# Kernel optimization log

Hardware: AMD Instinct MI355X
Metric: run time of the kernel (lower is better)

## Reference

```python
import jax, jax.numpy as jnp
import numpy as np

D_MODEL = 1024
N_HEADS = 16
D_K = D_MODEL // N_HEADS
MAX_REL = 128
SCALE = float(np.sqrt(D_K))


def setup_inputs() -> dict:
    key = jax.random.key(0)
    ks = jax.random.split(key, 10)
    B, S = 8, 1024
    return {
        "query": jax.random.normal(ks[0], (B, S, D_MODEL), jnp.float32),
        "key": jax.random.normal(ks[1], (B, S, D_MODEL), jnp.float32),
        "value": jax.random.normal(ks[2], (B, S, D_MODEL), jnp.float32),
        "w_q": jax.random.normal(ks[3], (D_MODEL, D_MODEL), jnp.float32) * (1.0 / np.sqrt(D_MODEL)),
        "w_k": jax.random.normal(ks[4], (D_MODEL, D_MODEL), jnp.float32) * (1.0 / np.sqrt(D_MODEL)),
        "w_v": jax.random.normal(ks[5], (D_MODEL, D_MODEL), jnp.float32) * (1.0 / np.sqrt(D_MODEL)),
        "w_o": jax.random.normal(ks[6], (D_MODEL, D_MODEL), jnp.float32) * (1.0 / np.sqrt(D_MODEL)),
        "b_o": jnp.zeros((D_MODEL,), jnp.float32),
        "rel_k": jax.random.normal(ks[7], (2 * MAX_REL + 1, D_K), jnp.float32),
        "rel_v": jax.random.normal(ks[8], (2 * MAX_REL + 1, D_K), jnp.float32),
        "temporal_decay": jnp.ones((N_HEADS,), jnp.float32),
    }


def reference(query, key, value, w_q, w_k, w_v, w_o, b_o, rel_k, rel_v, temporal_decay):
    B, S, D = query.shape
    H, dk = N_HEADS, D_K
    # projections (torch Linear: x @ W.T), reshape to [B,H,S,dk]
    def proj(x, W):
        return (x @ W.T).reshape(B, S, H, dk).transpose(0, 2, 1, 3)
    Q = proj(query, w_q)
    K = proj(key, w_k)
    V = proj(value, w_v)
    scores = jnp.einsum('bhld,bhrd->bhlr', Q, K) / SCALE
    # relative position indices [S,S] in [0, 2*MAX_REL]
    pos = jnp.arange(S)
    rel_idx = jnp.clip(pos[None, :] - pos[:, None], -MAX_REL, MAX_REL) + MAX_REL
    rp_k = rel_k[rel_idx]  # [S,S,dk]
    scores = scores + jnp.einsum('bhld,lrd->bhlr', Q, rp_k)
    # temporal decay bias
    time_dist = jnp.abs(pos[None, :] - pos[:, None]).astype(scores.dtype)  # [S,S]
    scores = scores - temporal_decay[None, :, None, None] * time_dist[None, None]
    attn = jax.nn.softmax(scores, axis=-1)
    context = jnp.einsum('bhlr,bhrd->bhld', attn, V)
    rp_v = rel_v[rel_idx]  # [S,S,dk]
    context = context + jnp.einsum('bhlr,lrd->bhld', attn, rp_v)
    context = context.transpose(0, 2, 1, 3).reshape(B, S, D)
    output = context @ w_o.T + b_o
    return output, attn
```

## Files before the change

### kernel.cpp

```cpp
#include <hip/hip_runtime.h>
#include <cstdint>
#include <cstddef>

#define S_LEN 1024
#define DMODEL 1024
#define NHEADS 16
#define DK 64
#define BATCH 8
#define PUS 296
#define PBS 272
#define RELS 257
#define SLABS 68

using half8_t  = __attribute__((ext_vector_type(8))) _Float16;
using half4_t  = __attribute__((ext_vector_type(4))) _Float16;
using float4_t = __attribute__((ext_vector_type(4))) float;

__device__ __forceinline__ void async16(const void* g, void* l) {
  __builtin_amdgcn_global_load_lds(
      (const __attribute__((address_space(1))) unsigned int*)g,
      (__attribute__((address_space(3))) unsigned int*)l, 16, 0, 0);
}

struct CvtRegion { const float* src; _Float16* dst; int n4; float scale; };
struct CvtArgs { CvtRegion r[8]; };

__global__ __launch_bounds__(256) void cvt_all_kernel(CvtArgs a) {
  CvtRegion reg = a.r[blockIdx.y];
  const int stride = gridDim.x * 256;
  for (int i = blockIdx.x * 256 + threadIdx.x; i < reg.n4; i += stride) {
    float4_t f = ((const float4_t*)reg.src)[i];
    half4_t h;
    h[0] = (_Float16)(f[0] * reg.scale); h[1] = (_Float16)(f[1] * reg.scale);
    h[2] = (_Float16)(f[2] * reg.scale); h[3] = (_Float16)(f[3] * reg.scale);
    ((half4_t*)reg.dst)[i] = h;
  }
}

__global__ void build_rvT_kernel(const float* __restrict__ relv, _Float16* __restrict__ rvT) {
  int d = blockIdx.x;
  int j = threadIdx.x;
  rvT[d * 256 + j] = (j < 255) ? (_Float16)relv[(size_t)(j + 1) * DK + d] : (_Float16)0.f;
}

__device__ __forceinline__ void gemm_core(
    const _Float16* __restrict__ A, const _Float16* __restrict__ B,
    _Float16* smem, float4_t acc[4][4], int m0, int n0,
    int wave, int lane, int quad, int ln, int wm, int wn)
{
  _Float16* As = smem;
  _Float16* Bs = smem + 8192;
#pragma unroll
  for (int i = 0; i < 4; i++)
#pragma unroll
    for (int j = 0; j < 4; j++) { acc[i][j][0]=0.f; acc[i][j][1]=0.f; acc[i][j][2]=0.f; acc[i][j][3]=0.f; }

  for (int k0 = 0; k0 < 1024; k0 += 64) {
#pragma unroll
    for (int q = 0; q < 4; q++) {
      int slot = q * 256 + wave * 64 + lane;
      int m = slot >> 3, g = slot & 7;
      int gg = g ^ (m & 7);
      async16(A + (size_t)(m0 + m) * 1024 + k0 + gg * 8,
              As + (size_t)(q * 256 + wave * 64) * 8);
      async16(B + (size_t)(n0 + m) * 1024 + k0 + gg * 8,
              Bs + (size_t)(q * 256 + wave * 64) * 8);
    }
    __syncthreads();
    half8_t af[4][2], bf[4][2];
#pragma unroll
    for (int t = 0; t < 4; t++) {
      int mm = wm + t * 16 + ln;
      int nn = wn + t * 16 + ln;
#pragma unroll
      for (int kk = 0; kk < 2; kk++) {
        af[t][kk] = *(const half8_t*)(As + mm * 64 + (((kk * 4 + quad) ^ (mm & 7)) * 8));
        bf[t][kk] = *(const half8_t*)(Bs + nn * 64 + (((kk * 4 + quad) ^ (nn & 7)) * 8));
      }
    }
#pragma unroll
    for (int i = 0; i < 4; i++)
#pragma unroll
      for (int j = 0; j < 4; j++) {
        acc[i][j] = __builtin_amdgcn_mfma_f32_16x16x32_f16(af[i][0], bf[j][0], acc[i][j], 0, 0, 0);
        acc[i][j] = __builtin_amdgcn_mfma_f32_16x16x32_f16(af[i][1], bf[j][1], acc[i][j], 0, 0, 0);
      }
    __syncthreads();
  }
}

struct QkvArgs {
  const _Float16* A[3];
  const _Float16* B[3];
  _Float16* dst[3];
};

__global__ __launch_bounds__(256) void gemm_qkv(QkvArgs qa) {
  __shared__ _Float16 smem[16384];
  const int tid = threadIdx.x;
  const int wave = tid >> 6, lane = tid & 63;
  const int quad = lane >> 4, ln = lane & 15;
  const int m0 = blockIdx.x * 128, n0 = blockIdx.y * 128;
  const int wm = (wave >> 1) * 64, wn = (wave & 1) * 64;
  const int z = blockIdx.z;

  float4_t acc[4][4];
  gemm_core(qa.A[z], qa.B[z], smem, acc, m0, n0, wave, lane, quad, ln, wm, wn);

  _Float16* o = qa.dst[z];
  if (z < 2) {
    _Float16* T = smem + wave * 1152;
    size_t headoff = ((size_t)((n0 + wn) >> 6)) << 16;
#pragma unroll
    for (int i = 0; i < 4; i++) {
#pragma unroll
      for (int j = 0; j < 4; j++)
#pragma unroll
        for (int r = 0; r < 4; r++)
          T[(quad * 4 + r) * 72 + j * 16 + ln] = (_Float16)acc[i][j][r];
      int mbase = m0 + wm + i * 16;
#pragma unroll
      for (int p = 0; p < 2; p++) {
        int row = p * 8 + (lane >> 3);
        int cc = (lane & 7) * 8;
        half8_t hv = *(const half8_t*)(T + row * 72 + cc);
        int token = mbase + row;
        size_t idx = ((size_t)(token >> 10) << 20) | headoff
                   | ((size_t)(token & 1023) << 6) | (size_t)cc;
        *(half8_t*)(o + idx) = hv;
      }
    }
  } else {
    _Float16* T = smem + wave * 1160;
    const int tok0 = m0 + wm;
    const size_t base = ((size_t)(tok0 >> 10) << 20)
                      | (((size_t)((n0 + wn) >> 6)) << 16)
                      | (size_t)(tok0 & 1023);
#pragma unroll
    for (int j = 0; j < 4; j++) {
#pragma unroll
      for (int i = 0; i < 4; i++)
#pragma unroll
        for (int r = 0; r < 4; r++)
          T[ln * 72 + i * 16 + quad * 4 + r] = (_Float16)acc[i][j][r];
#pragma unroll
      for (int p = 0; p < 2; p++) {
        int drow = p * 8 + (lane >> 3);
        int cc = (lane & 7) * 8;
        half8_t hv = *(const half8_t*)(T + drow * 72 + cc);
        size_t idx = base + (((size_t)(j * 16 + drow)) << 10) + (size_t)cc;
        *(half8_t*)(o + idx) = hv;
      }
    }
  }
}

__global__ __launch_bounds__(256) void gemm_out(
    const _Float16* __restrict__ A, const _Float16* __restrict__ B,
    float* __restrict__ o, const float* __restrict__ bias)
{
  __shared__ _Float16 smem[16384];
  const int tid = threadIdx.x;
  const int wave = tid >> 6, lane = tid & 63;
  const int quad = lane >> 4, ln = lane & 15;
  const int m0 = blockIdx.x * 128, n0 = blockIdx.y * 128;
  const int wm = (wave >> 1) * 64, wn = (wave & 1) * 64;

  float4_t acc[4][4];
  gemm_core(A, B, smem, acc, m0, n0, wave, lane, quad, ln, wm, wn);

#pragma unroll
  for (int i = 0; i < 4; i++)
#pragma unroll
    for (int j = 0; j < 4; j++) {
      int nn = n0 + wn + j * 16 + ln;
      float bb = bias[nn];
#pragma unroll
      for (int r = 0; r < 4; r++) {
        int mm = m0 + wm + i * 16 + quad * 4 + r;
        o[(size_t)mm * 1024 + nn] = acc[i][j][r] + bb;
      }
    }
}

__global__ __launch_bounds__(256, 4) void attn4_kernel(
    const _Float16* __restrict__ Qh, const _Float16* __restrict__ Kh,
    const _Float16* __restrict__ VtG, const _Float16* __restrict__ relk,
    const _Float16* __restrict__ rvT, const float* __restrict__ decay,
    float* __restrict__ attn_out, _Float16* __restrict__ ctx)
{
  __shared__ float    scratch[4 * 16 * SLABS];
  __shared__ _Float16 Pu[16 * PUS];
  __shared__ _Float16 Pband[16 * PBS];
  __shared__ float    statsM[4][16];
  __shared__ float    statsZ[4][16];

  const int tid = threadIdx.x;
  const int wave = tid >> 6, lane = tid & 63;
  const int quad = lane >> 4, ln = lane & 15;
  const int hw = blockIdx.x;
  const int bid = ((hw & 7) << 10) | (hw >> 3);
  const int b = bid >> 10, h = (bid >> 6) & 15, lt = bid & 63;
  const int l0 = lt * 16;
  const int bh = b * NHEADS + h;
  const _Float16* Qb = Qh + ((size_t)bh << 16);
  const _Float16* Kb = Kh + ((size_t)bh << 16);
  const _Float16* Vb = VtG + ((size_t)bh << 16);
  float* arow = attn_out + ((size_t)bh << 20) + (size_t)l0 * S_LEN;
  const float dec = decay[h];

  const int rlo = (l0 > 127) ? ((l0 - 127) & ~15) : 0;
  int rhi = (l0 + 158) & ~15;
  if (rhi > S_LEN) rhi = S_LEN;
  const int W = rhi - rlo;
  const int nT = W >> 4;
  const int ts = (wave * nT) >> 2;
  const int te = ((wave + 1) * nT) >> 2;

  const float4_t fz = {0.f, 0.f, 0.f, 0.f};
  {
    int w4l = rlo >> 2;
    int w4r = (S_LEN - rhi) >> 2;
#pragma unroll 1
    for (int row = 0; row < 16; row++) {
      float* ar = arow + (size_t)row * S_LEN;
      for (int c4 = tid; c4 < w4l; c4 += 256)
        __builtin_nontemporal_store(fz, (float4_t*)(ar + c4 * 4));
      float* ar2 = ar + rhi;
      for (int c4 = tid; c4 < w4r; c4 += 256)
        __builtin_nontemporal_store(fz, (float4_t*)(ar2 + c4 * 4));
    }
  }
  {
    const half8_t hz = {};
    for (int i = tid; i < 16 * PBS / 8; i += 256) ((half8_t*)Pband)[i] = hz;
    for (int i = tid; i < 16 * PUS / 8; i += 256) ((half8_t*)Pu)[i] = hz;
  }

  half8_t aq[2];
  {
    const _Float16* qp = Qb + (size_t)(l0 + ln) * DK + quad * 8;
    aq[0] = *(const half8_t*)(qp);
    aq[1] = *(const half8_t*)(qp + 32);
  }

#pragma unroll
  for (int s = 0; s < 4; s++) {
    int nt = wave * 4 + s;
    int j = nt * 16 + ln;
    const _Float16* bp = relk + (size_t)(j + 1) * DK + quad * 8;
    half8_t b0 = *(const half8_t*)bp;
    half8_t b1 = *(const half8_t*)(bp + 32);
    float4_t c = {0.f, 0.f, 0.f, 0.f};
    c = __builtin_amdgcn_mfma_f32_16x16x32_f16(aq[0], b0, c, 0, 0, 0);
    c = __builtin_amdgcn_mfma_f32_16x16x32_f16(aq[1], b1, c, 0, 0, 0);
    float db = dec * fabsf((float)(j - 127));
#pragma unroll
    for (int i = 0; i < 4; i++) scratch[(quad * 4 + i) * RELS + j] = c[i] - db;
  }
  __syncthreads();

  float4_t sreg[5];
#pragma unroll
  for (int tt = 0; tt < 5; tt++) { sreg[tt][0]=-1e30f; sreg[tt][1]=-1e30f; sreg[tt][2]=-1e30f; sreg[tt][3]=-1e30f; }

#pragma unroll
  for (int tt = 0; tt < 5; tt++) {
    int t = ts + tt;
    if (t < te) {
      int r0 = rlo + t * 16;
      const _Float16* kp = Kb + (size_t)(r0 + ln) * DK + quad * 8;
      half8_t b0 = *(const half8_t*)(kp);
      half8_t b1 = *(const half8_t*)(kp + 32);
      float4_t c = {0.f, 0.f, 0.f, 0.f};
      c = __builtin_amdgcn_mfma_f32_16x16x32_f16(aq[0], b0, c, 0, 0, 0);
      c = __builtin_amdgcn_mfma_f32_16x16x32_f16(aq[1], b1, c, 0, 0, 0);
      int r = r0 + ln;
#pragma unroll
      for (int i = 0; i < 4; i++) {
        int row = quad * 4 + i;
        int dd = r - (l0 + row);
        bool valid = (dd >= -127) && (dd <= 127);
        sreg[tt][i] = valid ? (c[i] + scratch[row * RELS + (dd + 127)]) : -1e30f;
      }
    }
  }

  float mw[4] = {-1e30f, -1e30f, -1e30f, -1e30f};
#pragma unroll
  for (int tt = 0; tt < 5; tt++)
#pragma unroll
    for (int i = 0; i < 4; i++) mw[i] = fmaxf(mw[i], sreg[tt][i]);
#pragma unroll
  for (int off = 1; off < 16; off <<= 1)
#pragma unroll
    for (int i = 0; i < 4; i++) mw[i] = fmaxf(mw[i], __shfl_xor(mw[i], off, 64));

  float ew[4] = {0.f, 0.f, 0.f, 0.f};
#pragma unroll
  for (int tt = 0; tt < 5; tt++)
#pragma unroll
    for (int i = 0; i < 4; i++) {
      float e = (sreg[tt][i] > -1e29f) ? __expf(sreg[tt][i] - mw[i]) : 0.f;
      sreg[tt][i] = e;
      ew[i] += e;
    }
#pragma unroll
  for (int off = 1; off < 16; off <<= 1)
#pragma unroll
    for (int i = 0; i < 4; i++) ew[i] += __shfl_xor(ew[i], off, 64);

  if (ln == 0) {
#pragma unroll
    for (int i = 0; i < 4; i++) {
      statsM[wave][quad * 4 + i] = mw[i];
      statsZ[wave][quad * 4 + i] = ew[i];
    }
  }
  __syncthreads();

  float scale[4];
#pragma unroll
  for (int i = 0; i < 4; i++) {
    int row = quad * 4 + i;
    float mf = fmaxf(fmaxf(statsM[0][row], statsM[1][row]),
                     fmaxf(statsM[2][row], statsM[3][row]));
    float z = statsZ[0][row] * __expf(statsM[0][row] - mf)
            + statsZ[1][row] * __expf(statsM[1][row] - mf)
            + statsZ[2][row] * __expf(statsM[2][row] - mf)
            + statsZ[3][row] * __expf(statsM[3][row] - mf);
    scale[i] = __expf(mw[i] - mf) / z;
  }

#pragma unroll
  for (int tt = 0; tt < 5; tt++) {
    int t = ts + tt;
    if (t < te) {
      int col = t * 16 + ln;
      int r = rlo + col;
#pragma unroll
      for (int i = 0; i < 4; i++) {
        int row = quad * 4 + i;
        _Float16 ph = (_Float16)(sreg[tt][i] * scale[i]);
        Pu[row * PUS + col] = ph;
        int dd = r - (l0 + row);
        if (dd >= -127 && dd <= 127) Pband[row * PBS + (dd + 127)] = ph;
      }
    }
  }
  __syncthreads();

  {
    int row = tid >> 4;
    int lc = tid & 15;
    float* ar = arow + (size_t)row * S_LEN + rlo;
    const _Float16* pr = Pu + row * PUS;
    int W4 = W >> 2;
    for (int c4 = lc; c4 < W4; c4 += 16) {
      half4_t hp = *(const half4_t*)(pr + c4 * 4);
      float4_t f;
      f[0] = (float)hp[0]; f[1] = (float)hp[1];
      f[2] = (float)hp[2]; f[3] = (float)hp[3];
      __builtin_nontemporal_store(f, (float4_t*)(ar + c4 * 4));
    }
  }

  float4_t ctxa[4];
#pragma unroll
  for (int nt = 0; nt < 4; nt++) { ctxa[nt][0]=0.f; ctxa[nt][1]=0.f; ctxa[nt][2]=0.f; ctxa[nt][3]=0.f; }
  {
    int nC = (W + 31) >> 5;
    int cs = (wave * nC) >> 2, ce = ((wave + 1) * nC) >> 2;
    for (int cc2 = cs; cc2 < ce; cc2++) {
      half8_t a = *(const half8_t*)(Pu + ln * PUS + cc2 * 32 + quad * 8);
      int rb = rlo + cc2 * 32 + quad * 8;
#pragma unroll
      for (int nt = 0; nt < 4; nt++) {
        half8_t bv = *(const half8_t*)(Vb + (size_t)(nt * 16 + ln) * S_LEN + rb);
        ctxa[nt] = __builtin_amdgcn_mfma_f32_16x16x32_f16(a, bv, ctxa[nt], 0, 0, 0);
      }
    }
  }

  {
    float4_t rc = {0.f, 0.f, 0.f, 0.f};
#pragma unroll
    for (int cch = 0; cch < 8; cch++) {
      half8_t apb = *(const half8_t*)(Pband + ln * PBS + cch * 32 + quad * 8);
      half8_t bb  = *(const half8_t*)(rvT + (size_t)(wave * 16 + ln) * 256 + cch * 32 + quad * 8);
      rc = __builtin_amdgcn_mfma_f32_16x16x32_f16(apb, bb, rc, 0, 0, 0);
    }
    if (wave == 0)      { ctxa[0][0]+=rc[0]; ctxa[0][1]+=rc[1]; ctxa[0][2]+=rc[2]; ctxa[0][3]+=rc[3]; }
    else if (wave == 1) { ctxa[1][0]+=rc[0]; ctxa[1][1]+=rc[1]; ctxa[1][2]+=rc[2]; ctxa[1][3]+=rc[3]; }
    else if (wave == 2) { ctxa[2][0]+=rc[0]; ctxa[2][1]+=rc[1]; ctxa[2][2]+=rc[2]; ctxa[2][3]+=rc[3]; }
    else                { ctxa[3][0]+=rc[0]; ctxa[3][1]+=rc[1]; ctxa[3][2]+=rc[2]; ctxa[3][3]+=rc[3]; }
  }

  {
    float* slab = scratch + wave * (16 * SLABS);
#pragma unroll
    for (int nt = 0; nt < 4; nt++)
#pragma unroll
      for (int i = 0; i < 4; i++)
        slab[(quad * 4 + i) * SLABS + nt * 16 + ln] = ctxa[nt][i];
  }
  __syncthreads();

  {
    int l = tid >> 4, d4 = (tid & 15) * 4;
    const float* s0 = scratch + l * SLABS + d4;
    float4_t v0 = *(const float4_t*)(s0);
    float4_t v1 = *(const float4_t*)(s0 + 16 * SLABS);
    float4_t v2 = *(const float4_t*)(s0 + 32 * SLABS);
    float4_t v3 = *(const float4_t*)(s0 + 48 * SLABS);
    half4_t hv;
    hv[0] = (_Float16)(v0[0] + v1[0] + v2[0] + v3[0]);
    hv[1] = (_Float16)(v0[1] + v1[1] + v2[1] + v3[1]);
    hv[2] = (_Float16)(v0[2] + v1[2] + v2[2] + v3[2]);
    hv[3] = (_Float16)(v0[3] + v1[3] + v2[3] + v3[3]);
    *(half4_t*)(ctx + ((size_t)(b * S_LEN + l0 + l)) * DMODEL + h * DK + d4) = hv;
  }
}

extern "C" void kernel_launch(void* const* d_in, const int* in_sizes, int n_in,
                              void* d_out, int out_size, void* d_ws, size_t ws_size,
                              hipStream_t stream) {
  const float* q   = (const float*)d_in[0];
  const float* k   = (const float*)d_in[1];
  const float* v   = (const float*)d_in[2];
  const float* wq  = (const float*)d_in[3];
  const float* wk  = (const float*)d_in[4];
  const float* wv  = (const float*)d_in[5];
  const float* wo  = (const float*)d_in[6];
  const float* bo  = (const float*)d_in[7];
  const float* rk  = (const float*)d_in[8];
  const float* rv  = (const float*)d_in[9];
  const float* td  = (const float*)d_in[10];

  char* ws = (char*)d_ws;
  size_t off = 0;
  auto alloc = [&](size_t bytes) -> void* {
    void* p = ws + off;
    off += (bytes + 255) & ~(size_t)255;
    return p;
  };
  const size_t NTOK = (size_t)BATCH * S_LEN;
  _Float16* Xq  = (_Float16*)alloc(NTOK * DMODEL * 2);
  _Float16* Xk  = (_Float16*)alloc(NTOK * DMODEL * 2);
  _Float16* Xv  = (_Float16*)alloc(NTOK * DMODEL * 2);
  _Float16* Wqh = (_Float16*)alloc((size_t)DMODEL * DMODEL * 2);
  _Float16* Wkh = (_Float16*)alloc((size_t)DMODEL * DMODEL * 2);
  _Float16* Wvh = (_Float16*)alloc((size_t)DMODEL * DMODEL * 2);
  _Float16* Woh = (_Float16*)alloc((size_t)DMODEL * DMODEL * 2);
  _Float16* Qh  = (_Float16*)alloc(NTOK * DMODEL * 2);
  _Float16* Kh  = (_Float16*)alloc(NTOK * DMODEL * 2);
  _Float16* VtG = (_Float16*)alloc(NTOK * DMODEL * 2 + 256);
  _Float16* Ctx = (_Float16*)alloc(NTOK * DMODEL * 2);
  _Float16* Rkh = (_Float16*)alloc((size_t)257 * 64 * 2);
  _Float16* RvT = (_Float16*)alloc((size_t)64 * 256 * 2);

  CvtArgs ca;
  ca.r[0] = {q,  Xq,  (int)(NTOK * DMODEL / 4), 1.f};
  ca.r[1] = {k,  Xk,  (int)(NTOK * DMODEL / 4), 1.f};
  ca.r[2] = {v,  Xv,  (int)(NTOK * DMODEL / 4), 1.f};
  ca.r[3] = {wq, Wqh, DMODEL * DMODEL / 4, 0.125f};
  ca.r[4] = {wk, Wkh, DMODEL * DMODEL / 4, 1.f};
  ca.r[5] = {wv, Wvh, DMODEL * DMODEL / 4, 1.f};
  ca.r[6] = {wo, Woh, DMODEL * DMODEL / 4, 1.f};
  ca.r[7] = {rk, Rkh, 257 * 64 / 4, 8.f};
  cvt_all_kernel<<<dim3(512, 8), dim3(256), 0, stream>>>(ca);
  build_rvT_kernel<<<dim3(64), dim3(256), 0, stream>>>(rv, RvT);

  QkvArgs qa;
  qa.A[0] = Xq; qa.A[1] = Xk; qa.A[2] = Xv;
  qa.B[0] = Wqh; qa.B[1] = Wkh; qa.B[2] = Wvh;
  qa.dst[0] = Qh; qa.dst[1] = Kh; qa.dst[2] = VtG;
  gemm_qkv<<<dim3(64, 8, 3), dim3(256), 0, stream>>>(qa);

  float* attn_out = (float*)d_out + NTOK * DMODEL;
  attn4_kernel<<<dim3(BATCH * NHEADS * (S_LEN / 16)), dim3(256), 0, stream>>>(
      Qh, Kh, VtG, Rkh, RvT, td, attn_out, Ctx);

  gemm_out<<<dim3(64, 8), dim3(256), 0, stream>>>(Ctx, Woh, (float*)d_out, bo);
}
```

Measured before the change: 793.8 us.

## Process 32 query rows per attention block with two wave groups

The attention kernel now handles a 32-row query tile per 512-thread block instead of 16 rows per 256 threads. Waves are split into two row groups that share the same K/V band window and the same rel-V tile. The intent is to cut redundant global loads of K, V and the relative tables across neighbouring query tiles, and to halve the number of blocks. In exchange each block needs more LDS and registers, and the launch bound of 512 threads with 4 blocks may limit occupancy.

```diff
diff --git a/kernel.cpp b/kernel.cpp
--- a/kernel.cpp
+++ b/kernel.cpp
@@ -7,6 +7,7 @@
 #define NHEADS 16
 #define DK 64
 #define BATCH 8
+#define QBLK 32
 #define PUS 296
 #define PBS 272
 #define RELS 257
@@ -183,25 +184,27 @@
     }
 }
 
-__global__ __launch_bounds__(256, 4) void attn4_kernel(
+__global__ __launch_bounds__(512, 4) void attn4_kernel(
     const _Float16* __restrict__ Qh, const _Float16* __restrict__ Kh,
     const _Float16* __restrict__ VtG, const _Float16* __restrict__ relk,
     const _Float16* __restrict__ rvT, const float* __restrict__ decay,
     float* __restrict__ attn_out, _Float16* __restrict__ ctx)
 {
-  __shared__ float    scratch[4 * 16 * SLABS];
-  __shared__ _Float16 Pu[16 * PUS];
-  __shared__ _Float16 Pband[16 * PBS];
-  __shared__ float    statsM[4][16];
-  __shared__ float    statsZ[4][16];
+  __shared__ float    scratch[8 * 16 * SLABS];
+  __shared__ _Float16 Pu[QBLK * PUS];
+  __shared__ _Float16 Pband[QBLK * PBS];
+  __shared__ float    statsM[2][4][16];
+  __shared__ float    statsZ[2][4][16];
 
   const int tid = threadIdx.x;
   const int wave = tid >> 6, lane = tid & 63;
   const int quad = lane >> 4, ln = lane & 15;
+  const int rg = wave >> 2;
+  const int wg = wave & 3;
   const int hw = blockIdx.x;
-  const int bid = ((hw & 7) << 10) | (hw >> 3);
-  const int b = bid >> 10, h = (bid >> 6) & 15, lt = bid & 63;
-  const int l0 = lt * 16;
+  const int bid = ((hw & 7) << 9) | (hw >> 3);
+  const int b = bid >> 9, h = (bid >> 5) & 15, lt = bid & 31;
+  const int l0 = lt * QBLK;
   const int bh = b * NHEADS + h;
   const _Float16* Qb = Qh + ((size_t)bh << 16);
   const _Float16* Kb = Kh + ((size_t)bh << 16);
@@ -210,43 +213,43 @@
   const float dec = decay[h];
 
   const int rlo = (l0 > 127) ? ((l0 - 127) & ~15) : 0;
-  int rhi = (l0 + 158) & ~15;
+  int rhi = (l0 + QBLK + 142) & ~15;
   if (rhi > S_LEN) rhi = S_LEN;
   const int W = rhi - rlo;
   const int nT = W >> 4;
-  const int ts = (wave * nT) >> 2;
-  const int te = ((wave + 1) * nT) >> 2;
+  const int ts = (wg * nT) >> 2;
+  const int te = ((wg + 1) * nT) >> 2;
 
   const float4_t fz = {0.f, 0.f, 0.f, 0.f};
   {
     int w4l = rlo >> 2;
     int w4r = (S_LEN - rhi) >> 2;
 #pragma unroll 1
-    for (int row = 0; row < 16; row++) {
+    for (int row = 0; row < QBLK; row++) {
       float* ar = arow + (size_t)row * S_LEN;
-      for (int c4 = tid; c4 < w4l; c4 += 256)
+      for (int c4 = tid; c4 < w4l; c4 += 512)
         __builtin_nontemporal_store(fz, (float4_t*)(ar + c4 * 4));
       float* ar2 = ar + rhi;
-      for (int c4 = tid; c4 < w4r; c4 += 256)
+      for (int c4 = tid; c4 < w4r; c4 += 512)
         __builtin_nontemporal_store(fz, (float4_t*)(ar2 + c4 * 4));
     }
   }
   {
     const half8_t hz = {};
-    for (int i = tid; i < 16 * PBS / 8; i += 256) ((half8_t*)Pband)[i] = hz;
-    for (int i = tid; i < 16 * PUS / 8; i += 256) ((half8_t*)Pu)[i] = hz;
+    for (int i = tid; i < QBLK * PBS / 8; i += 512) ((half8_t*)Pband)[i] = hz;
+    for (int i = tid; i < QBLK * PUS / 8; i += 512) ((half8_t*)Pu)[i] = hz;
   }
 
   half8_t aq[2];
   {
-    const _Float16* qp = Qb + (size_t)(l0 + ln) * DK + quad * 8;
+    const _Float16* qp = Qb + (size_t)(l0 + rg * 16 + ln) * DK + quad * 8;
     aq[0] = *(const half8_t*)(qp);
     aq[1] = *(const half8_t*)(qp + 32);
   }
 
 #pragma unroll
   for (int s = 0; s < 4; s++) {
-    int nt = wave * 4 + s;
+    int nt = wg * 4 + s;
     int j = nt * 16 + ln;
     const _Float16* bp = relk + (size_t)(j + 1) * DK + quad * 8;
     half8_t b0 = *(const half8_t*)bp;
@@ -256,7 +259,8 @@
     c = __builtin_amdgcn_mfma_f32_16x16x32_f16(aq[1], b1, c, 0, 0, 0);
     float db = dec * fabsf((float)(j - 127));
 #pragma unroll
-    for (int i = 0; i < 4; i++) scratch[(quad * 4 + i) * RELS + j] = c[i] - db;
+    for (int i = 0; i < 4; i++)
+      scratch[(rg * 16 + quad * 4 + i) * RELS + j] = c[i] - db;
   }
   __syncthreads();
 
@@ -278,7 +282,7 @@
       int r = r0 + ln;
 #pragma unroll
       for (int i = 0; i < 4; i++) {
-        int row = quad * 4 + i;
+        int row = rg * 16 + quad * 4 + i;
         int dd = r - (l0 + row);
         bool valid = (dd >= -127) && (dd <= 127);
         sreg[tt][i] = valid ? (c[i] + scratch[row * RELS + (dd + 127)]) : -1e30f;
@@ -313,8 +317,8 @@
   if (ln == 0) {
 #pragma unroll
     for (int i = 0; i < 4; i++) {
-      statsM[wave][quad * 4 + i] = mw[i];
-      statsZ[wave][quad * 4 + i] = ew[i];
+      statsM[rg][wg][quad * 4 + i] = mw[i];
+      statsZ[rg][wg][quad * 4 + i] = ew[i];
     }
   }
   __syncthreads();
@@ -322,13 +326,13 @@
   float scale[4];
 #pragma unroll
   for (int i = 0; i < 4; i++) {
-    int row = quad * 4 + i;
-    float mf = fmaxf(fmaxf(statsM[0][row], statsM[1][row]),
-                     fmaxf(statsM[2][row], statsM[3][row]));
-    float z = statsZ[0][row] * __expf(statsM[0][row] - mf)
-            + statsZ[1][row] * __expf(statsM[1][row] - mf)
-            + statsZ[2][row] * __expf(statsM[2][row] - mf)
-            + statsZ[3][row] * __expf(statsM[3][row] - mf);
+    int r16 = quad * 4 + i;
+    float mf = fmaxf(fmaxf(statsM[rg][0][r16], statsM[rg][1][r16]),
+                     fmaxf(statsM[rg][2][r16], statsM[rg][3][r16]));
+    float z = statsZ[rg][0][r16] * __expf(statsM[rg][0][r16] - mf)
+            + statsZ[rg][1][r16] * __expf(statsM[rg][1][r16] - mf)
+            + statsZ[rg][2][r16] * __expf(statsM[rg][2][r16] - mf)
+            + statsZ[rg][3][r16] * __expf(statsM[rg][3][r16] - mf);
     scale[i] = __expf(mw[i] - mf) / z;
   }
 
@@ -340,7 +344,7 @@
       int r = rlo + col;
 #pragma unroll
       for (int i = 0; i < 4; i++) {
-        int row = quad * 4 + i;
+        int row = rg * 16 + quad * 4 + i;
         _Float16 ph = (_Float16)(sreg[tt][i] * scale[i]);
         Pu[row * PUS + col] = ph;
         int dd = r - (l0 + row);
@@ -370,9 +374,9 @@
   for (int nt = 0; nt < 4; nt++) { ctxa[nt][0]=0.f; ctxa[nt][1]=0.f; ctxa[nt][2]=0.f; ctxa[nt][3]=0.f; }
   {
     int nC = (W + 31) >> 5;
-    int cs = (wave * nC) >> 2, ce = ((wave + 1) * nC) >> 2;
+    int cs = (wg * nC) >> 2, ce = ((wg + 1) * nC) >> 2;
     for (int cc2 = cs; cc2 < ce; cc2++) {
-      half8_t a = *(const half8_t*)(Pu + ln * PUS + cc2 * 32 + quad * 8);
+      half8_t a = *(const half8_t*)(Pu + (rg * 16 + ln) * PUS + cc2 * 32 + quad * 8);
       int rb = rlo + cc2 * 32 + quad * 8;
 #pragma unroll
       for (int nt = 0; nt < 4; nt++) {
@@ -386,14 +390,14 @@
     float4_t rc = {0.f, 0.f, 0.f, 0.f};
 #pragma unroll
     for (int cch = 0; cch < 8; cch++) {
-      half8_t apb = *(const half8_t*)(Pband + ln * PBS + cch * 32 + quad * 8);
-      half8_t bb  = *(const half8_t*)(rvT + (size_t)(wave * 16 + ln) * 256 + cch * 32 + quad * 8);
+      half8_t apb = *(const half8_t*)(Pband + (rg * 16 + ln) * PBS + cch * 32 + quad * 8);
+      half8_t bb  = *(const half8_t*)(rvT + (size_t)(wg * 16 + ln) * 256 + cch * 32 + quad * 8);
       rc = __builtin_amdgcn_mfma_f32_16x16x32_f16(apb, bb, rc, 0, 0, 0);
     }
-    if (wave == 0)      { ctxa[0][0]+=rc[0]; ctxa[0][1]+=rc[1]; ctxa[0][2]+=rc[2]; ctxa[0][3]+=rc[3]; }
-    else if (wave == 1) { ctxa[1][0]+=rc[0]; ctxa[1][1]+=rc[1]; ctxa[1][2]+=rc[2]; ctxa[1][3]+=rc[3]; }
-    else if (wave == 2) { ctxa[2][0]+=rc[0]; ctxa[2][1]+=rc[1]; ctxa[2][2]+=rc[2]; ctxa[2][3]+=rc[3]; }
-    else                { ctxa[3][0]+=rc[0]; ctxa[3][1]+=rc[1]; ctxa[3][2]+=rc[2]; ctxa[3][3]+=rc[3]; }
+    if (wg == 0)      { ctxa[0][0]+=rc[0]; ctxa[0][1]+=rc[1]; ctxa[0][2]+=rc[2]; ctxa[0][3]+=rc[3]; }
+    else if (wg == 1) { ctxa[1][0]+=rc[0]; ctxa[1][1]+=rc[1]; ctxa[1][2]+=rc[2]; ctxa[1][3]+=rc[3]; }
+    else if (wg == 2) { ctxa[2][0]+=rc[0]; ctxa[2][1]+=rc[1]; ctxa[2][2]+=rc[2]; ctxa[2][3]+=rc[3]; }
+    else              { ctxa[3][0]+=rc[0]; ctxa[3][1]+=rc[1]; ctxa[3][2]+=rc[2]; ctxa[3][3]+=rc[3]; }
   }
 
   {
@@ -408,7 +412,8 @@
 
   {
     int l = tid >> 4, d4 = (tid & 15) * 4;
-    const float* s0 = scratch + l * SLABS + d4;
+    int g = l >> 4, lrow = l & 15;
+    const float* s0 = scratch + (size_t)(g * 4) * (16 * SLABS) + lrow * SLABS + d4;
     float4_t v0 = *(const float4_t*)(s0);
     float4_t v1 = *(const float4_t*)(s0 + 16 * SLABS);
     float4_t v2 = *(const float4_t*)(s0 + 32 * SLABS);
@@ -478,7 +483,7 @@
   gemm_qkv<<<dim3(64, 8, 3), dim3(256), 0, stream>>>(qa);
 
   float* attn_out = (float*)d_out + NTOK * DMODEL;
-  attn4_kernel<<<dim3(BATCH * NHEADS * (S_LEN / 16)), dim3(256), 0, stream>>>(
+  attn4_kernel<<<dim3(BATCH * NHEADS * (S_LEN / QBLK)), dim3(512), 0, stream>>>(
       Qh, Kh, VtG, Rkh, RvT, td, attn_out, Ctx);
 
   gemm_out<<<dim3(64, 8), dim3(256), 0, stream>>>(Ctx, Woh, (float*)d_out, bo);
```

Result: no change. 796.3 us (+0.3%).
